# Optimization experiments

Hardware: AMD Instinct MI355X
Metric: run time of the kernel (lower is better)

The kernel has to match this reference:

```python
import jax, jax.numpy as jnp
import numpy as np

B, N, C = 64, 1024, 128


def setup_inputs() -> dict:
    key = jax.random.key(0)
    k1, k2, k3, k4, k5, k6 = jax.random.split(key, 6)
    adj_vals = jax.random.uniform(k1, (B, N, N), dtype=jnp.float32)
    mask = jax.random.uniform(k2, (B, N, N)) < 0.1
    adjacent = jnp.where(mask, adj_vals, 0.0)
    annotations = jax.random.normal(k3, (B, N, C), dtype=jnp.float32)
    # GraphConvolution bias, shape (1,1,C)
    gc_bias = jax.random.normal(k4, (1, 1, C), dtype=jnp.float32) * 0.05
    # Keras GRU params (reset_after=True default): kernel (C,3C), recurrent (C,3C), bias (2,3C)
    kernel = jax.random.normal(k5, (C, 3 * C), dtype=jnp.float32) / np.sqrt(C)
    recurrent_kernel = jax.random.normal(k6, (C, 3 * C), dtype=jnp.float32) / np.sqrt(C)
    gru_bias = jnp.zeros((2, 3 * C), dtype=jnp.float32)
    return {"adjacent": adjacent, "annotations": annotations, "gc_bias": gc_bias,
            "kernel": kernel, "recurrent_kernel": recurrent_kernel, "gru_bias": gru_bias}


def reference(adjacent, annotations, gc_bias, kernel, recurrent_kernel, gru_bias):
    # GraphConvolution: per-graph adj @ annotations, batched, + bias
    v = jnp.einsum('bij,bjc->bic', adjacent, annotations) + gc_bias  # [B,N,C]
    b, n, c = v.shape
    x = v.reshape(-1, c)            # visible states, one GRU step each
    h = annotations.reshape(-1, c)  # initial hidden states
    # single-step Keras GRU (reset_after=True)
    mx = x @ kernel + gru_bias[0]
    mh = h @ recurrent_kernel + gru_bias[1]
    xz, xr, xh = jnp.split(mx, 3, axis=-1)
    hz, hr, hh_in = jnp.split(mh, 3, axis=-1)
    z = jax.nn.sigmoid(xz + hz)
    r = jax.nn.sigmoid(xr + hr)
    hh = jnp.tanh(xh + r * hh_in)
    out = z * h + (1.0 - z) * hh
    return out.reshape(b, n, c)
```

## Files before the change

### kernel.cpp

```cpp
#include <hip/hip_runtime.h>

typedef unsigned short ushort_t;
typedef __attribute__((ext_vector_type(8))) short bf16x8;
typedef __attribute__((ext_vector_type(8))) unsigned short u16x8;
typedef __attribute__((ext_vector_type(4))) float f32x4;

#define B_ 64
#define N_ 1024
#define C_ 128

static __device__ __forceinline__ unsigned short f2bf(float f) {
  union { float f; unsigned int i; } v; v.f = f;
  unsigned int i = v.i;
  return (unsigned short)((i + 0x7FFFu + ((i >> 16) & 1u)) >> 16);
}
static __device__ __forceinline__ void split1(float x, ushort_t& h, ushort_t& l) {
  union { float f; unsigned int i; } u; u.f = x;
  h = (ushort_t)(u.i >> 16);
  union { unsigned int i; float f; } t; t.i = u.i & 0xFFFF0000u;
  union { float f; unsigned int i; } w; w.f = x - t.f;
  l = (ushort_t)(w.i >> 16);
}
static __device__ __forceinline__ bf16x8 as_bf(u16x8 v) {
  union { u16x8 u; bf16x8 b; } x; x.u = v; return x.b;
}
static __device__ __forceinline__ void gload_lds16(const void* g, void* l) {
  __builtin_amdgcn_global_load_lds((const __attribute__((address_space(1))) void*)g,
                                   (__attribute__((address_space(3))) void*)l,
                                   16, 0, 0);
}

#define PIPE_BAR(N) asm volatile("s_waitcnt vmcnt(" #N ")\n\ts_barrier" ::: "memory")
#define POST_BAR()  asm volatile("s_waitcnt lgkmcnt(0)\n\ts_barrier" ::: "memory")

__global__ __launch_bounds__(256) void tsplit(const float* __restrict__ src,
                                              ushort_t* __restrict__ dh,
                                              ushort_t* __restrict__ dl,
                                              int rows, int cols, long sb, long db) {
  __shared__ float tile[64][65];
  const int t = threadIdx.x;
  src += (long)blockIdx.z * sb;
  dh  += (long)blockIdx.z * db;
  dl  += (long)blockIdx.z * db;
  const int r0 = blockIdx.y * 64, c0 = blockIdx.x * 64;
#pragma unroll
  for (int p = 0; p < 4; ++p) {
    int row = p * 16 + (t >> 4), c4 = (t & 15) * 4;
    f32x4 v = *(const f32x4*)(src + (long)(r0 + row) * cols + c0 + c4);
#pragma unroll
    for (int j = 0; j < 4; ++j) tile[row][c4 + j] = v[j];
  }
  __syncthreads();
  const int oc = t >> 2;
#pragma unroll
  for (int p = 0; p < 2; ++p) {
    int ck = (t & 3) + p * 4;
    u16x8 vh, vl;
#pragma unroll
    for (int j = 0; j < 8; ++j) {
      ushort_t hj, lj;
      split1(tile[ck * 8 + j][oc], hj, lj);
      vh[j] = hj; vl[j] = lj;
    }
    long o = (long)(c0 + oc) * rows + r0 + ck * 8;
    *(u16x8*)(dh + o) = vh;
    *(u16x8*)(dl + o) = vl;
  }
}

__global__ __launch_bounds__(256, 2) void gc_gemm(const float* __restrict__ adj,
                                                  const ushort_t* __restrict__ annTh,
                                                  const ushort_t* __restrict__ annTl,
                                                  const float* __restrict__ gcb,
                                                  float* __restrict__ vout) {
  __shared__ __align__(16) float lds_all[2 * 8192];

  const int tid = threadIdx.x;
  const int w = tid >> 6, lane = tid & 63;
  const int wr = w >> 1, wc = w & 1;
  const int swz = (blockIdx.x & 7) * 64 + (blockIdx.x >> 3);
  const int b = swz >> 3;
  const int m0 = (swz & 7) * 128;

  const float*    adjb = adj   + ((long)b * N_ + m0) * N_;
  const ushort_t* aThb = annTh + (long)b * C_ * N_;
  const ushort_t* aTlb = annTl + (long)b * C_ * N_;

  const int fr = lane & 15;
  const int kg = lane >> 4;
  const int aRow = lane >> 3;
  const int aCs  = (lane & 7) ^ aRow;
  const int bRow = lane >> 2;
  const int bCs  = (lane & 3) ^ ((lane >> 3) & 3);

  f32x4 acc[4][4] = {};

#define STAGE(Q, T)                                                            \
  {                                                                            \
    const int k0_ = (T) * 32;                                                  \
    float*    A_  = lds_all + (Q) * 8192;                                      \
    ushort_t* Bh_ = (ushort_t*)(lds_all + (Q) * 8192 + 4096);                  \
    ushort_t* Bl_ = (ushort_t*)(lds_all + (Q) * 8192 + 6144);                  \
    _Pragma("unroll")                                                          \
    for (int jj = 0; jj < 4; ++jj) {                                           \
      int j_ = w * 4 + jj;                                                     \
      gload_lds16(adjb + (long)(j_ * 8 + aRow) * N_ + k0_ + aCs * 4,           \
                  (void*)(A_ + j_ * 256));                                     \
    }                                                                          \
    _Pragma("unroll")                                                          \
    for (int jj = 0; jj < 2; ++jj) {                                           \
      int j_ = w * 2 + jj;                                                     \
      long so_ = (long)(j_ * 16 + bRow) * N_ + k0_ + bCs * 8;                  \
      gload_lds16(aThb + so_, (void*)(Bh_ + j_ * 512));                        \
      gload_lds16(aTlb + so_, (void*)(Bl_ + j_ * 512));                        \
    }                                                                          \
  }

#define COMPUTE(Q)                                                             \
  {                                                                            \
    const float*    A_  = lds_all + (Q) * 8192;                                \
    const ushort_t* Bh_ = (const ushort_t*)(lds_all + (Q) * 8192 + 4096);      \
    const ushort_t* Bl_ = (const ushort_t*)(lds_all + (Q) * 8192 + 6144);      \
    bf16x8 bh_[4], bl_[4], ah_[4], al_[4];                                     \
    _Pragma("unroll")                                                          \
    for (int ni = 0; ni < 4; ++ni) {                                           \
      int row_ = wc * 64 + ni * 16 + fr;                                       \
      int kb_ = (kg << 4) ^ ((((row_) >> 1) & 3) << 4);                        \
      bh_[ni] = *(const bf16x8*)((const char*)Bh_ + row_ * 64 + kb_);          \
      bl_[ni] = *(const bf16x8*)((const char*)Bl_ + row_ * 64 + kb_);          \
    }                                                                          \
    _Pragma("unroll")                                                          \
    for (int mi = 0; mi < 4; ++mi) {                                           \
      int row_ = wr * 64 + mi * 16 + fr;                                       \
      int b0_ = row_ * 128 + ((kg * 32) ^ ((row_ & 7) << 4));                  \
      f32x4 a0_ = *(const f32x4*)((const char*)A_ + b0_);                      \
      f32x4 a1_ = *(const f32x4*)((const char*)A_ + (b0_ ^ 16));               \
      u16x8 vh_, vl_;                                                          \
      _Pragma("unroll")                                                        \
      for (int j = 0; j < 4; ++j) {                                            \
        ushort_t hj_, lj_;                                                     \
        split1(a0_[j], hj_, lj_); vh_[j] = hj_;     vl_[j] = lj_;              \
        split1(a1_[j], hj_, lj_); vh_[4 + j] = hj_; vl_[4 + j] = lj_;          \
      }                                                                        \
      ah_[mi] = as_bf(vh_); al_[mi] = as_bf(vl_);                              \
    }                                                                          \
    _Pragma("unroll")                                                          \
    for (int mi = 0; mi < 4; ++mi)                                             \
      _Pragma("unroll")                                                        \
      for (int ni = 0; ni < 4; ++ni) {                                         \
        acc[mi][ni] = __builtin_amdgcn_mfma_f32_16x16x32_bf16(ah_[mi], bh_[ni], acc[mi][ni], 0, 0, 0); \
        acc[mi][ni] = __builtin_amdgcn_mfma_f32_16x16x32_bf16(al_[mi], bh_[ni], acc[mi][ni], 0, 0, 0); \
        acc[mi][ni] = __builtin_amdgcn_mfma_f32_16x16x32_bf16(ah_[mi], bl_[ni], acc[mi][ni], 0, 0, 0); \
      }                                                                        \
  }

  STAGE(0, 0)
#pragma unroll 1
  for (int t = 0; t < 31; ++t) {
    const int cur = t & 1;
    STAGE(cur ^ 1, t + 1)
    PIPE_BAR(8);
    COMPUTE(cur)
    POST_BAR();
  }
  PIPE_BAR(0);
  COMPUTE(1)

  const long rowbase = (long)b * N_ + m0 + wr * 64;
#pragma unroll
  for (int ni = 0; ni < 4; ++ni) {
    int col = wc * 64 + ni * 16 + fr;
    float bias = gcb[col];
#pragma unroll
    for (int mi = 0; mi < 4; ++mi)
#pragma unroll
      for (int r = 0; r < 4; ++r)
        vout[(rowbase + mi * 16 + kg * 4 + r) * C_ + col] = acc[mi][ni][r] + bias;
  }
#undef STAGE
#undef COMPUTE
}

__global__ __launch_bounds__(256, 1) void gru(const float* __restrict__ v,
                                              const float* __restrict__ ann,
                                              const ushort_t* __restrict__ kTh,
                                              const ushort_t* __restrict__ kTl,
                                              const ushort_t* __restrict__ rTh,
                                              const float* __restrict__ gb,
                                              float* __restrict__ out) {
  const int w = threadIdx.x >> 6, lane = threadIdx.x & 63;
  const long m0 = ((long)blockIdx.x * 4 + w) * 32;
  const int fr = lane & 15, kg = lane >> 4;

  bf16x8 xh[2][4], xl[2][4], hh[2][4];
#pragma unroll
  for (int s = 0; s < 2; ++s)
#pragma unroll
    for (int kk = 0; kk < 4; ++kk) {
      long off = (m0 + s * 16 + fr) * (long)C_ + kk * 32 + kg * 8;
      f32x4 x0 = *(const f32x4*)(v + off);
      f32x4 x1 = *(const f32x4*)(v + off + 4);
      u16x8 th, tl;
#pragma unroll
      for (int j = 0; j < 4; ++j) {
        ushort_t hj, lj;
        split1(x0[j], hj, lj); th[j] = hj; tl[j] = lj;
        split1(x1[j], hj, lj); th[4 + j] = hj; tl[4 + j] = lj;
      }
      xh[s][kk] = as_bf(th); xl[s][kk] = as_bf(tl);
      f32x4 h0 = *(const f32x4*)(ann + off);
      f32x4 h1 = *(const f32x4*)(ann + off + 4);
      u16x8 hv;
#pragma unroll
      for (int j = 0; j < 4; ++j) { hv[j] = f2bf(h0[j]); hv[4 + j] = f2bf(h1[j]); }
      hh[s][kk] = as_bf(hv);
    }

  bf16x8 WK[4], WL[4], WR[4];
  float HV[8];

#define LOADW(NN, GG)                                                          \
  {                                                                            \
    const ushort_t* kh_ = kTh + (long)((GG) * C_ + (NN) * 16 + fr) * C_;       \
    const ushort_t* kl_ = kTl + (long)((GG) * C_ + (NN) * 16 + fr) * C_;       \
    const ushort_t* rh_ = rTh + (long)((GG) * C_ + (NN) * 16 + fr) * C_;       \
    _Pragma("unroll")                                                          \
    for (int kk = 0; kk < 4; ++kk) {                                           \
      int o_ = kk * 32 + kg * 8;                                               \
      WK[kk] = *(const bf16x8*)(kh_ + o_);                                     \
      WL[kk] = *(const bf16x8*)(kl_ + o_);                                     \
      WR[kk] = *(const bf16x8*)(rh_ + o_);                                     \
    }                                                                          \
  }

#define MATH(AK0, AK1, AR0, AR1)                                               \
  {                                                                            \
    _Pragma("unroll")                                                          \
    for (int kk = 0; kk < 4; ++kk) {                                           \
      AK0 = __builtin_amdgcn_mfma_f32_16x16x32_bf16(xh[0][kk], WK[kk], AK0, 0, 0, 0); \
      AK1 = __builtin_amdgcn_mfma_f32_16x16x32_bf16(xh[1][kk], WK[kk], AK1, 0, 0, 0); \
      AK0 = __builtin_amdgcn_mfma_f32_16x16x32_bf16(xl[0][kk], WK[kk], AK0, 0, 0, 0); \
      AK1 = __builtin_amdgcn_mfma_f32_16x16x32_bf16(xl[1][kk], WK[kk], AK1, 0, 0, 0); \
      AK0 = __builtin_amdgcn_mfma_f32_16x16x32_bf16(xh[0][kk], WL[kk], AK0, 0, 0, 0); \
      AK1 = __builtin_amdgcn_mfma_f32_16x16x32_bf16(xh[1][kk], WL[kk], AK1, 0, 0, 0); \
    }                                                                          \
    _Pragma("unroll")                                                          \
    for (int kk = 0; kk < 4; ++kk) {                                           \
      AR0 = __builtin_amdgcn_mfma_f32_16x16x32_bf16(hh[0][kk], WR[kk], AR0, 0, 0, 0); \
      AR1 = __builtin_amdgcn_mfma_f32_16x16x32_bf16(hh[1][kk], WR[kk], AR1, 0, 0, 0); \
    }                                                                          \
  }

#pragma unroll 1
  for (int n = 0; n < 8; ++n) {
    f32x4 az0 = {}, az1 = {}, ar0 = {}, ar1 = {}, ax0 = {}, ax1 = {}, ah0 = {}, ah1 = {};
    LOADW(n, 0)
    MATH(az0, az1, az0, az1)
    LOADW(n, 1)
    MATH(ar0, ar1, ar0, ar1)
    LOADW(n, 2)
    MATH(ax0, ax1, ah0, ah1)

    const int cb = n * 16 + fr;
#pragma unroll
    for (int s = 0; s < 2; ++s)
#pragma unroll
      for (int r = 0; r < 4; ++r)
        HV[s * 4 + r] = ann[(m0 + s * 16 + kg * 4 + r) * (long)C_ + cb];

    const float bz  = gb[cb] + gb[384 + cb];
    const float brr = gb[128 + cb] + gb[384 + 128 + cb];
    const float bxh = gb[256 + cb];
    const float bhi = gb[384 + 256 + cb];
#pragma unroll
    for (int s = 0; s < 2; ++s) {
      const f32x4& az_ = s ? az1 : az0;
      const f32x4& ar_ = s ? ar1 : ar0;
      const f32x4& ax_ = s ? ax1 : ax0;
      const f32x4& ah_ = s ? ah1 : ah0;
#pragma unroll
      for (int r = 0; r < 4; ++r) {
        long row = m0 + s * 16 + kg * 4 + r;
        float hval = HV[s * 4 + r];
        float zz = 1.f / (1.f + __expf(-(az_[r] + bz)));
        float rr = 1.f / (1.f + __expf(-(ar_[r] + brr)));
        float hpre = ax_[r] + bxh + rr * (ah_[r] + bhi);
        hpre = fminf(fmaxf(hpre, -15.f), 15.f);
        float e2 = __expf(2.f * hpre);
        float th = (e2 - 1.f) / (e2 + 1.f);
        out[row * C_ + cb] = zz * hval + (1.f - zz) * th;
      }
    }
  }
#undef LOADW
#undef MATH
}

extern "C" void kernel_launch(void* const* d_in, const int* in_sizes, int n_in,
                              void* d_out, int out_size, void* d_ws, size_t ws_size,
                              hipStream_t stream) {
  const float* adj = (const float*)d_in[0];
  const float* ann = (const float*)d_in[1];
  const float* gcb = (const float*)d_in[2];
  const float* ker = (const float*)d_in[3];
  const float* rk  = (const float*)d_in[4];
  const float* gb  = (const float*)d_in[5];
  float* out = (float*)d_out;

  char* ws = (char*)d_ws;
  ushort_t* annTh = (ushort_t*)(ws);
  ushort_t* annTl = (ushort_t*)(ws + 16777216);
  ushort_t* kTh   = (ushort_t*)(ws + 33554432);
  ushort_t* kTl   = (ushort_t*)(ws + 33652736);
  ushort_t* rTh   = (ushort_t*)(ws + 33751040);
  ushort_t* rTl   = (ushort_t*)(ws + 33849344);
  float*    vbuf  = (float*)(ws + 33947648);

  hipLaunchKernelGGL(tsplit, dim3(2, 16, 64), dim3(256), 0, stream,
                     ann, annTh, annTl, 1024, 128, (long)1024 * 128, (long)128 * 1024);
  hipLaunchKernelGGL(tsplit, dim3(6, 2, 1), dim3(256), 0, stream,
                     ker, kTh, kTl, 128, 384, 0L, 0L);
  hipLaunchKernelGGL(tsplit, dim3(6, 2, 1), dim3(256), 0, stream,
                     rk, rTh, rTl, 128, 384, 0L, 0L);
  hipLaunchKernelGGL(gc_gemm, dim3(512), dim3(256), 0, stream,
                     adj, annTh, annTl, gcb, vbuf);
  hipLaunchKernelGGL(gru, dim3(512), dim3(256), 0, stream,
                     vbuf, ann, kTh, kTl, rTh, gb, out);
}
```

Before: 183.9 us.

## Stage GRU weight slices through swizzled LDS shared by eight waves

The GRU kernel now uses 512-thread blocks in which each wave handles 16 rows instead of 32. Each 16-column weight slice (kernel hi/lo and recurrent hi) is loaded once per block into XOR-swizzled shared memory, with the next slice prefetched into registers while the current one is consumed. Previously every wave read the weights directly from global memory. The change is meant to cut redundant global/L2 weight traffic and raise occupancy through smaller per-wave register state, at the cost of two barriers per slice iteration.

```diff
diff --git a/kernel.cpp b/kernel.cpp
--- a/kernel.cpp
+++ b/kernel.cpp
@@ -181,118 +181,145 @@
 #undef COMPUTE
 }
 
-__global__ __launch_bounds__(256, 1) void gru(const float* __restrict__ v,
+__global__ __launch_bounds__(512, 4) void gru(const float* __restrict__ v,
                                               const float* __restrict__ ann,
                                               const ushort_t* __restrict__ kTh,
                                               const ushort_t* __restrict__ kTl,
                                               const ushort_t* __restrict__ rTh,
                                               const float* __restrict__ gb,
                                               float* __restrict__ out) {
-  const int w = threadIdx.x >> 6, lane = threadIdx.x & 63;
-  const long m0 = ((long)blockIdx.x * 4 + w) * 32;
+  __shared__ __align__(16) ushort_t wlds[18432];
+
+  const int tid = threadIdx.x;
+  const int w = tid >> 6, lane = tid & 63;
+  const long m0 = (long)blockIdx.x * 128 + w * 16;
   const int fr = lane & 15, kg = lane >> 4;
-
-  bf16x8 xh[2][4], xl[2][4], hh[2][4];
-#pragma unroll
-  for (int s = 0; s < 2; ++s)
-#pragma unroll
-    for (int kk = 0; kk < 4; ++kk) {
-      long off = (m0 + s * 16 + fr) * (long)C_ + kk * 32 + kg * 8;
-      f32x4 x0 = *(const f32x4*)(v + off);
-      f32x4 x1 = *(const f32x4*)(v + off + 4);
-      u16x8 th, tl;
-#pragma unroll
-      for (int j = 0; j < 4; ++j) {
-        ushort_t hj, lj;
-        split1(x0[j], hj, lj); th[j] = hj; tl[j] = lj;
-        split1(x1[j], hj, lj); th[4 + j] = hj; tl[4 + j] = lj;
-      }
-      xh[s][kk] = as_bf(th); xl[s][kk] = as_bf(tl);
-      f32x4 h0 = *(const f32x4*)(ann + off);
-      f32x4 h1 = *(const f32x4*)(ann + off + 4);
-      u16x8 hv;
-#pragma unroll
-      for (int j = 0; j < 4; ++j) { hv[j] = f2bf(h0[j]); hv[4 + j] = f2bf(h1[j]); }
-      hh[s][kk] = as_bf(hv);
+  const int frk = fr & 7;
+
+  bf16x8 xh[4], xl[4], hh[4];
+#pragma unroll
+  for (int kk = 0; kk < 4; ++kk) {
+    long off = (m0 + fr) * (long)C_ + kk * 32 + kg * 8;
+    f32x4 x0 = *(const f32x4*)(v + off);
+    f32x4 x1 = *(const f32x4*)(v + off + 4);
+    u16x8 th, tl;
+#pragma unroll
+    for (int j = 0; j < 4; ++j) {
+      ushort_t hj, lj;
+      split1(x0[j], hj, lj); th[j] = hj; tl[j] = lj;
+      split1(x1[j], hj, lj); th[4 + j] = hj; tl[4 + j] = lj;
     }
-
-  bf16x8 WK[4], WL[4], WR[4];
-  float HV[8];
-
-#define LOADW(NN, GG)                                                          \
-  {                                                                            \
-    const ushort_t* kh_ = kTh + (long)((GG) * C_ + (NN) * 16 + fr) * C_;       \
-    const ushort_t* kl_ = kTl + (long)((GG) * C_ + (NN) * 16 + fr) * C_;       \
-    const ushort_t* rh_ = rTh + (long)((GG) * C_ + (NN) * 16 + fr) * C_;       \
+    xh[kk] = as_bf(th); xl[kk] = as_bf(tl);
+    f32x4 h0 = *(const f32x4*)(ann + off);
+    f32x4 h1 = *(const f32x4*)(ann + off + 4);
+    u16x8 hv;
+#pragma unroll
+    for (int j = 0; j < 4; ++j) { hv[j] = f2bf(h0[j]); hv[4 + j] = f2bf(h1[j]); }
+    hh[kk] = as_bf(hv);
+  }
+
+  const ushort_t* wsrc[5];
+  int wdst[5];
+#pragma unroll
+  for (int q = 0; q < 5; ++q) {
+    int c = tid + q * 512;
+    int cc = (c < 2304) ? c : 0;
+    int arr = cc / 768, rem = cc % 768;
+    int gate = rem >> 8, rem2 = rem & 255, row = rem2 >> 4, sp = rem2 & 15;
+    int ssrc = sp ^ (row & 7);
+    const ushort_t* base = (arr == 0) ? kTh : ((arr == 1) ? kTl : rTh);
+    wsrc[q] = base + (gate * 128 + row) * 128 + ssrc * 8;
+    wdst[q] = cc * 16;
+  }
+  const bool act4 = (tid < 256);
+
+  u16x8 wreg0, wreg1, wreg2, wreg3, wreg4;
+
+#define LOADWREG(NN)                                                           \
+  {                                                                            \
+    wreg0 = *(const u16x8*)(wsrc[0] + (NN) * 2048);                            \
+    wreg1 = *(const u16x8*)(wsrc[1] + (NN) * 2048);                            \
+    wreg2 = *(const u16x8*)(wsrc[2] + (NN) * 2048);                            \
+    wreg3 = *(const u16x8*)(wsrc[3] + (NN) * 2048);                            \
+    if (act4) wreg4 = *(const u16x8*)(wsrc[4] + (NN) * 2048);                  \
+  }
+
+#define DSWRITE()                                                              \
+  {                                                                            \
+    *(u16x8*)((char*)wlds + wdst[0]) = wreg0;                                  \
+    *(u16x8*)((char*)wlds + wdst[1]) = wreg1;                                  \
+    *(u16x8*)((char*)wlds + wdst[2]) = wreg2;                                  \
+    *(u16x8*)((char*)wlds + wdst[3]) = wreg3;                                  \
+    if (act4) *(u16x8*)((char*)wlds + wdst[4]) = wreg4;                        \
+  }
+
+#define WOFF(A, G, KK) (((((A) * 3 + (G)) * 16 + fr) * 16 + (((KK) * 4 + kg) ^ frk)) * 16)
+
+#define MATH(G, AK, AR)                                                        \
+  {                                                                            \
+    bf16x8 KH[4], KL[4], RH[4];                                                \
     _Pragma("unroll")                                                          \
     for (int kk = 0; kk < 4; ++kk) {                                           \
-      int o_ = kk * 32 + kg * 8;                                               \
-      WK[kk] = *(const bf16x8*)(kh_ + o_);                                     \
-      WL[kk] = *(const bf16x8*)(kl_ + o_);                                     \
-      WR[kk] = *(const bf16x8*)(rh_ + o_);                                     \
-    }                                                                          \
-  }
-
-#define MATH(AK0, AK1, AR0, AR1)                                               \
-  {                                                                            \
+      KH[kk] = *(const bf16x8*)((const char*)wlds + WOFF(0, G, kk));           \
+      KL[kk] = *(const bf16x8*)((const char*)wlds + WOFF(1, G, kk));           \
+      RH[kk] = *(const bf16x8*)((const char*)wlds + WOFF(2, G, kk));           \
+    }                                                                          \
     _Pragma("unroll")                                                          \
     for (int kk = 0; kk < 4; ++kk) {                                           \
-      AK0 = __builtin_amdgcn_mfma_f32_16x16x32_bf16(xh[0][kk], WK[kk], AK0, 0, 0, 0); \
-      AK1 = __builtin_amdgcn_mfma_f32_16x16x32_bf16(xh[1][kk], WK[kk], AK1, 0, 0, 0); \
-      AK0 = __builtin_amdgcn_mfma_f32_16x16x32_bf16(xl[0][kk], WK[kk], AK0, 0, 0, 0); \
-      AK1 = __builtin_amdgcn_mfma_f32_16x16x32_bf16(xl[1][kk], WK[kk], AK1, 0, 0, 0); \
-      AK0 = __builtin_amdgcn_mfma_f32_16x16x32_bf16(xh[0][kk], WL[kk], AK0, 0, 0, 0); \
-      AK1 = __builtin_amdgcn_mfma_f32_16x16x32_bf16(xh[1][kk], WL[kk], AK1, 0, 0, 0); \
+      AK = __builtin_amdgcn_mfma_f32_16x16x32_bf16(xh[kk], KH[kk], AK, 0, 0, 0); \
+      AK = __builtin_amdgcn_mfma_f32_16x16x32_bf16(xl[kk], KH[kk], AK, 0, 0, 0); \
+      AK = __builtin_amdgcn_mfma_f32_16x16x32_bf16(xh[kk], KL[kk], AK, 0, 0, 0); \
     }                                                                          \
     _Pragma("unroll")                                                          \
     for (int kk = 0; kk < 4; ++kk) {                                           \
-      AR0 = __builtin_amdgcn_mfma_f32_16x16x32_bf16(hh[0][kk], WR[kk], AR0, 0, 0, 0); \
-      AR1 = __builtin_amdgcn_mfma_f32_16x16x32_bf16(hh[1][kk], WR[kk], AR1, 0, 0, 0); \
-    }                                                                          \
-  }
+      AR = __builtin_amdgcn_mfma_f32_16x16x32_bf16(hh[kk], RH[kk], AR, 0, 0, 0); \
+    }                                                                          \
+  }
+
+  LOADWREG(0)
+  DSWRITE()
+  __syncthreads();
 
 #pragma unroll 1
   for (int n = 0; n < 8; ++n) {
-    f32x4 az0 = {}, az1 = {}, ar0 = {}, ar1 = {}, ax0 = {}, ax1 = {}, ah0 = {}, ah1 = {};
-    LOADW(n, 0)
-    MATH(az0, az1, az0, az1)
-    LOADW(n, 1)
-    MATH(ar0, ar1, ar0, ar1)
-    LOADW(n, 2)
-    MATH(ax0, ax1, ah0, ah1)
+    if (n < 7) LOADWREG(n + 1)
+
+    f32x4 az = {}, ar = {}, ax = {}, ah = {};
+    MATH(0, az, az)
+    MATH(1, ar, ar)
+    MATH(2, ax, ah)
 
     const int cb = n * 16 + fr;
-#pragma unroll
-    for (int s = 0; s < 2; ++s)
-#pragma unroll
-      for (int r = 0; r < 4; ++r)
-        HV[s * 4 + r] = ann[(m0 + s * 16 + kg * 4 + r) * (long)C_ + cb];
+    float HV[4];
+#pragma unroll
+    for (int r = 0; r < 4; ++r)
+      HV[r] = ann[(m0 + kg * 4 + r) * (long)C_ + cb];
 
     const float bz  = gb[cb] + gb[384 + cb];
     const float brr = gb[128 + cb] + gb[384 + 128 + cb];
     const float bxh = gb[256 + cb];
     const float bhi = gb[384 + 256 + cb];
 #pragma unroll
-    for (int s = 0; s < 2; ++s) {
-      const f32x4& az_ = s ? az1 : az0;
-      const f32x4& ar_ = s ? ar1 : ar0;
-      const f32x4& ax_ = s ? ax1 : ax0;
-      const f32x4& ah_ = s ? ah1 : ah0;
-#pragma unroll
-      for (int r = 0; r < 4; ++r) {
-        long row = m0 + s * 16 + kg * 4 + r;
-        float hval = HV[s * 4 + r];
-        float zz = 1.f / (1.f + __expf(-(az_[r] + bz)));
-        float rr = 1.f / (1.f + __expf(-(ar_[r] + brr)));
-        float hpre = ax_[r] + bxh + rr * (ah_[r] + bhi);
-        hpre = fminf(fmaxf(hpre, -15.f), 15.f);
-        float e2 = __expf(2.f * hpre);
-        float th = (e2 - 1.f) / (e2 + 1.f);
-        out[row * C_ + cb] = zz * hval + (1.f - zz) * th;
-      }
+    for (int r = 0; r < 4; ++r) {
+      long row = m0 + kg * 4 + r;
+      float zz = 1.f / (1.f + __expf(-(az[r] + bz)));
+      float rr = 1.f / (1.f + __expf(-(ar[r] + brr)));
+      float hpre = ax[r] + bxh + rr * (ah[r] + bhi);
+      hpre = fminf(fmaxf(hpre, -15.f), 15.f);
+      float e2 = __expf(2.f * hpre);
+      float th = (e2 - 1.f) / (e2 + 1.f);
+      out[row * C_ + cb] = zz * HV[r] + (1.f - zz) * th;
     }
-  }
-#undef LOADW
+
+    if (n < 7) {
+      __syncthreads();
+      DSWRITE()
+      __syncthreads();
+    }
+  }
+#undef LOADWREG
+#undef DSWRITE
+#undef WOFF
 #undef MATH
 }
 
@@ -324,6 +351,6 @@
                      rk, rTh, rTl, 128, 384, 0L, 0L);
   hipLaunchKernelGGL(gc_gemm, dim3(512), dim3(256), 0, stream,
                      adj, annTh, annTl, gcb, vbuf);
-  hipLaunchKernelGGL(gru, dim3(512), dim3(256), 0, stream,
+  hipLaunchKernelGGL(gru, dim3(512), dim3(512), 0, stream,
                      vbuf, ann, kTh, kTl, rTh, gb, out);
 }
```

Result: slower. 192.4 us (+4.6%).
